# Optimization experiments

Hardware: AMD Instinct MI355X
Metric: run time of the kernel (lower is better)

The kernel has to match this reference:

```python
import jax, jax.numpy as jnp
import numpy as np

B, N, C = 2, 9216, 512
HEAD, SR = 8, 4
R = 32  # lora rank
SCALING = 4.0 / 32.0  # alpha / r


def setup_inputs() -> dict:
    key = jax.random.key(0)
    ks = jax.random.split(key, 16)
    s = 0.02
    inp = {
        "x": jax.random.normal(ks[0], (B, N, C), jnp.float32),
        "w_q": jax.random.normal(ks[1], (C, C), jnp.float32) * s,
        "b_q": jnp.zeros((C,), jnp.float32),
        "w_kv": jax.random.normal(ks[2], (2 * C, C), jnp.float32) * s,
        "b_kv": jnp.zeros((2 * C,), jnp.float32),
        "w_proj": jax.random.normal(ks[3], (C, C), jnp.float32) * s,
        "b_proj": jnp.zeros((C,), jnp.float32),
        "w_sr": jax.random.normal(ks[4], (C, C, SR, SR), jnp.float32) * s,
        "b_sr": jnp.zeros((C,), jnp.float32),
        "ln_g": jnp.ones((C,), jnp.float32),
        "ln_b": jnp.zeros((C,), jnp.float32),
        "lora_A_q": jax.random.normal(ks[5], (R, C), jnp.float32) * s,
        "lora_B_q": jax.random.normal(ks[6], (C, R), jnp.float32) * s,
        "lora_A_v": jax.random.normal(ks[7], (R, C), jnp.float32) * s,
        "lora_B_v": jax.random.normal(ks[8], (C, R), jnp.float32) * s,
        "H": 96,
        "W": 96,
    }
    return inp


def reference(x, w_q, b_q, w_kv, b_kv, w_proj, b_proj, w_sr, b_sr,
              ln_g, ln_b, lora_A_q, lora_B_q, lora_A_v, lora_B_v, H, W):
    b, n, c = x.shape
    d = c // HEAD
    # q = Linear(x) + LoRA(x) * scaling
    q = x @ w_q.T + b_q + ((x @ lora_A_q.T) @ lora_B_q.T) * SCALING
    q = q.reshape(b, n, HEAD, d).transpose(0, 2, 1, 3)  # (B, h, N, d)
    # spatial reduction: Conv2d(dim, dim, sr, sr) then LayerNorm
    xi = x.transpose(0, 2, 1).reshape(b, c, H, W)
    xs = jax.lax.conv_general_dilated(
        xi, w_sr, window_strides=(SR, SR), padding='VALID',
        dimension_numbers=('NCHW', 'OIHW', 'NCHW'))
    xs = xs + b_sr[None, :, None, None]
    xs = xs.reshape(b, c, -1).transpose(0, 2, 1)  # (B, Nkv, C)
    mu = jnp.mean(xs, axis=-1, keepdims=True)
    var = jnp.var(xs, axis=-1, keepdims=True)
    xs = (xs - mu) * jax.lax.rsqrt(var + 1e-5) * ln_g + ln_b
    # k, v
    kv = (xs @ w_kv.T + b_kv).reshape(b, -1, 2, HEAD, d).transpose(2, 0, 3, 1, 4)
    k, v = kv[0], kv[1]  # (B, h, Nkv, d)
    lv = ((xs @ lora_A_v.T) @ lora_B_v.T) * SCALING  # (B, Nkv, C)
    # faithful to torch: raw memory reshape, NOT a head-transpose
    v = v + lv.reshape(b, HEAD, -1, d)
    # attention
    attn = jax.nn.softmax(jnp.einsum('bhnd,bhmd->bhnm', q, k) * (d ** -0.5), axis=-1)
    out = jnp.einsum('bhnm,bhmd->bhnd', attn, v).transpose(0, 2, 1, 3).reshape(b, n, c)
    return out @ w_proj.T + b_proj
```

## Files before the change

### kernel.cpp

```cpp
#include <hip/hip_runtime.h>

typedef __attribute__((ext_vector_type(8))) __bf16 bf16x8;
typedef __attribute__((ext_vector_type(4))) float f32x4;
typedef __attribute__((ext_vector_type(4))) unsigned int u32x4;

#define MFMA16(a, b, c) __builtin_amdgcn_mfma_f32_16x16x32_bf16((a), (b), (c), 0, 0, 0)

__device__ __forceinline__ bool input_is_f32(const void* ln_g) {
    return ((const unsigned*)ln_g)[0] == 0x3F800000u;
}

__device__ __forceinline__ float rdf(const void* p, long i, bool f32) {
    return f32 ? ((const float*)p)[i] : (float)((const __bf16*)p)[i];
}

__device__ __forceinline__ void conv_big(const void* s, __bf16* d, long base, bool f) {
    long i = base + (long)threadIdx.x * 8;
    if (f) {
        f32x4 a = ((const f32x4*)s)[i / 4];
        f32x4 b = ((const f32x4*)s)[i / 4 + 1];
        bf16x8 o;
        #pragma unroll
        for (int j = 0; j < 4; ++j) { o[j] = (__bf16)a[j]; o[4 + j] = (__bf16)b[j]; }
        *(bf16x8*)(d + i) = o;
    } else {
        *(u32x4*)(d + i) = ((const u32x4*)s)[i / 8];
    }
}

__device__ __forceinline__ void conv_small(const void* s, __bf16* d, int n, bool f) {
    int i = threadIdx.x * 4;
    if (i < n) {
        #pragma unroll
        for (int j = 0; j < 4; ++j)
            d[i + j] = f ? (__bf16)((const float*)s)[i + j] : ((const __bf16*)s)[i + j];
    }
}

__global__ void convert_kernel(const void* x, const void* w_kv, const void* w_proj,
                               const void* b_q, const void* b_kv, const void* b_proj,
                               const void* b_sr, const void* ln_g, const void* ln_b,
                               __bf16* x_b, __bf16* w_kv_b, __bf16* w_proj_b,
                               __bf16* b_q_b, __bf16* b_kv_b, __bf16* b_proj_b,
                               __bf16* b_sr_b, __bf16* ln_g_b, __bf16* ln_b_b) {
    const bool f = input_is_f32(ln_g);
    int blk = blockIdx.x;
    if (blk < 4608)      conv_big(x, x_b, (long)blk * 2048, f);
    else if (blk < 4864) conv_big(w_kv, w_kv_b, (long)(blk - 4608) * 2048, f);
    else if (blk < 4992) conv_big(w_proj, w_proj_b, (long)(blk - 4864) * 2048, f);
    else if (blk == 4992) conv_small(b_q, b_q_b, 512, f);
    else if (blk == 4993) conv_small(b_kv, b_kv_b, 1024, f);
    else if (blk == 4994) conv_small(b_proj, b_proj_b, 512, f);
    else if (blk == 4995) conv_small(b_sr, b_sr_b, 512, f);
    else if (blk == 4996) conv_small(ln_g, ln_g_b, 512, f);
    else                  conv_small(ln_b, ln_b_b, 512, f);
}

__global__ void prep_kernel(const void* __restrict__ w_q,
                            const void* __restrict__ Aq, const void* __restrict__ Bq,
                            const void* __restrict__ Av, const void* __restrict__ Bv,
                            const void* __restrict__ w_sr, const void* __restrict__ ln_g,
                            __bf16* __restrict__ w_q_eff, __bf16* __restrict__ w_lv,
                            __bf16* __restrict__ w_sr_t) {
    const bool f = input_is_f32(ln_g);
    int tid = blockIdx.x * 256 + threadIdx.x;
    if (tid < 262144) {
        int o = tid >> 9, c = tid & 511;
        float acc = 0.f;
        #pragma unroll 8
        for (int r = 0; r < 32; ++r)
            acc += rdf(Bq, o * 32 + r, f) * rdf(Aq, r * 512 + c, f);
        w_q_eff[tid] = (__bf16)(rdf(w_q, tid, f) + 0.125f * acc);
    } else if (tid < 524288) {
        int t = tid - 262144;
        int o = t >> 9, c = t & 511;
        float acc = 0.f;
        #pragma unroll 8
        for (int r = 0; r < 32; ++r)
            acc += rdf(Bv, o * 32 + r, f) * rdf(Av, r * 512 + c, f);
        w_lv[t] = (__bf16)(0.125f * acc);
    } else if (tid < 786432) {
        int t = tid - 524288;
        int o = t >> 9, i = t & 511;
        #pragma unroll
        for (int p = 0; p < 16; ++p)
            w_sr_t[(size_t)o * 8192 + p * 512 + i] = (__bf16)rdf(w_sr, (long)t * 16 + p, f);
    }
}

__global__ __launch_bounds__(256) void gemm128(const __bf16* __restrict__ A,
                                               const __bf16* __restrict__ Bt,
                                               const __bf16* __restrict__ bias,
                                               void* __restrict__ out, int mode) {
    __shared__ __attribute__((aligned(16))) char lds[16384];
    char* As = lds;
    char* Bs = lds + 8192;
    const int tid = threadIdx.x;
    const int m0 = blockIdx.x << 7, n0 = blockIdx.y << 7;
    const int w = tid >> 6, lane = tid & 63;
    const int wm = (w >> 1) << 6, wn = (w & 1) << 6;
    const int lr = lane & 15, lg = lane >> 4;

    f32x4 acc[4][4] = {};

    const int srow = tid >> 1;
    const int sc0 = (tid & 1) * 2;
    const __bf16* Arow = A + (size_t)(m0 + srow) * 512;
    const __bf16* Brow = Bt + (size_t)(n0 + srow) * 512;

    for (int k0 = 0; k0 < 512; k0 += 32) {
        u32x4 a0 = *(const u32x4*)(Arow + k0 + sc0 * 8);
        u32x4 a1 = *(const u32x4*)(Arow + k0 + sc0 * 8 + 8);
        u32x4 b0 = *(const u32x4*)(Brow + k0 + sc0 * 8);
        u32x4 b1 = *(const u32x4*)(Brow + k0 + sc0 * 8 + 8);
        __syncthreads();
        *(u32x4*)(As + srow * 64 + sc0 * 16) = a0;
        *(u32x4*)(As + srow * 64 + sc0 * 16 + 16) = a1;
        *(u32x4*)(Bs + srow * 64 + sc0 * 16) = b0;
        *(u32x4*)(Bs + srow * 64 + sc0 * 16 + 16) = b1;
        __syncthreads();
        bf16x8 a[4], b[4];
        #pragma unroll
        for (int i = 0; i < 4; ++i)
            a[i] = *(const bf16x8*)(As + (wm + i * 16 + lr) * 64 + lg * 16);
        #pragma unroll
        for (int j = 0; j < 4; ++j)
            b[j] = *(const bf16x8*)(Bs + (wn + j * 16 + lr) * 64 + lg * 16);
        #pragma unroll
        for (int i = 0; i < 4; ++i)
            #pragma unroll
            for (int j = 0; j < 4; ++j)
                acc[i][j] = MFMA16(a[i], b[j], acc[i][j]);
    }

    #pragma unroll
    for (int j = 0; j < 4; ++j) {
        int col = n0 + wn + j * 16 + lr;
        float bv = (float)bias[col];
        #pragma unroll
        for (int i = 0; i < 4; ++i) {
            int rb = m0 + wm + i * 16 + lg * 4;
            #pragma unroll
            for (int r = 0; r < 4; ++r) {
                float v = acc[i][j][r] + bv;
                int grow = rb + r;
                if (mode == 0) {
                    ((float*)out)[(size_t)grow * 512 + col] = v;
                } else {
                    int b_ = grow >= 9216 ? 1 : 0;
                    int nn = grow - b_ * 9216;
                    ((__bf16*)out)[(((size_t)(b_ * 8 + (col >> 6))) * 9216 + nn) * 64 +
                                   (col & 63)] = (__bf16)v;
                }
            }
        }
    }
}

__global__ __launch_bounds__(256) void conv_gemm(const __bf16* __restrict__ x,
                                                 const __bf16* __restrict__ Wt,
                                                 float* __restrict__ part) {
    __shared__ __attribute__((aligned(16))) char lds[18432];
    char* As = lds;
    char* Bs = lds + 9216;
    const int tid = threadIdx.x;
    const int m0 = blockIdx.x << 6, n0 = blockIdx.y << 6;
    const int kz = blockIdx.z;
    const int kbase = kz << 10;
    const int w = tid >> 6, lane = tid & 63;
    const int wm = (w >> 1) << 5, wn = (w & 1) << 5;
    const int lr = lane & 15, lg = lane >> 4;

    const int srow = tid >> 2, sc = tid & 3;
    int m = m0 + srow;
    int bb = m >= 576 ? 1 : 0;
    int rem = m - bb * 576;
    int oy = rem / 24;
    int ox = rem - oy * 24;
    const __bf16* xrow = x + ((size_t)bb * 9216 + oy * 384 + ox * 4) * 512;
    const __bf16* brow = Wt + (size_t)(n0 + srow) * 8192;

    f32x4 acc[2][2] = {};
    for (int kk = 0; kk < 1024; kk += 64) {
        int k0 = kbase + kk;
        int p = k0 >> 9;
        int i0 = k0 & 511;
        int ky = p >> 2, kx = p & 3;
        const __bf16* xsrc = xrow + ((ky * 96 + kx) << 9) + i0;
        __syncthreads();
        #pragma unroll
        for (int j = 0; j < 2; ++j) {
            int c = sc + j * 4;
            u32x4 av = *(const u32x4*)(xsrc + c * 8);
            u32x4 bv = *(const u32x4*)(brow + k0 + c * 8);
            *(u32x4*)(As + srow * 144 + c * 16) = av;
            *(u32x4*)(Bs + srow * 144 + c * 16) = bv;
        }
        __syncthreads();
        bf16x8 a[2][2], b[2][2];
        #pragma unroll
        for (int i = 0; i < 2; ++i)
            #pragma unroll
            for (int ks = 0; ks < 2; ++ks) {
                a[i][ks] = *(const bf16x8*)(As + (wm + i * 16 + lr) * 144 + ks * 64 + lg * 16);
                b[i][ks] = *(const bf16x8*)(Bs + (wn + i * 16 + lr) * 144 + ks * 64 + lg * 16);
            }
        #pragma unroll
        for (int i = 0; i < 2; ++i)
            #pragma unroll
            for (int j = 0; j < 2; ++j)
                #pragma unroll
                for (int ks = 0; ks < 2; ++ks)
                    acc[i][j] = MFMA16(a[i][ks], b[j][ks], acc[i][j]);
    }
    float* pout = part + (size_t)kz * 589824;
    #pragma unroll
    for (int j = 0; j < 2; ++j) {
        int col = n0 + wn + j * 16 + lr;
        #pragma unroll
        for (int i = 0; i < 2; ++i) {
            int rb = m0 + wm + i * 16 + lg * 4;
            #pragma unroll
            for (int r = 0; r < 4; ++r)
                pout[(size_t)(rb + r) * 512 + col] = acc[i][j][r];
        }
    }
}

__global__ __launch_bounds__(64) void lnorm(const float* __restrict__ parts,
                                            const __bf16* __restrict__ b_sr,
                                            const __bf16* __restrict__ g,
                                            const __bf16* __restrict__ be,
                                            __bf16* __restrict__ out) {
    int row = blockIdx.x;
    int lane = threadIdx.x;
    const float* xr = parts + (size_t)row * 512;
    float v[8], s = 0.f, sq = 0.f;
    #pragma unroll
    for (int i = 0; i < 8; ++i) {
        int c = lane + i * 64;
        float t = (float)b_sr[c];
        #pragma unroll
        for (int sp = 0; sp < 8; ++sp)
            t += xr[(size_t)sp * 589824 + c];
        v[i] = t;
        s += t;
        sq += t * t;
    }
    #pragma unroll
    for (int d = 1; d < 64; d <<= 1) {
        s += __shfl_xor(s, d);
        sq += __shfl_xor(sq, d);
    }
    float mean = s * (1.0f / 512.0f);
    float var = sq * (1.0f / 512.0f) - mean * mean;
    float rstd = rsqrtf(var + 1e-5f);
    __bf16* orow = out + (size_t)row * 512;
    #pragma unroll
    for (int i = 0; i < 8; ++i) {
        int c = lane + i * 64;
        orow[c] = (__bf16)((v[i] - mean) * rstd * (float)g[c] + (float)be[c]);
    }
}

__global__ __launch_bounds__(256) void kv_gemm(const __bf16* __restrict__ xs,
                                               const __bf16* __restrict__ w_kv,
                                               const __bf16* __restrict__ w_lv,
                                               const __bf16* __restrict__ b_kv,
                                               __bf16* __restrict__ k_t,
                                               float* __restrict__ v_raw,
                                               __bf16* __restrict__ lv) {
    __shared__ __attribute__((aligned(16))) char lds[18432];
    char* As = lds;
    char* Bs = lds + 9216;
    const int tid = threadIdx.x;
    const int m0 = blockIdx.x << 6, n0 = blockIdx.y << 6;
    const int w = tid >> 6, lane = tid & 63;
    const int wm = (w >> 1) << 5, wn = (w & 1) << 5;
    const int lr = lane & 15, lg = lane >> 4;

    const int srow = tid >> 2, sc = tid & 3;
    const __bf16* arow = xs + (size_t)(m0 + srow) * 512;
    const __bf16* brow = (n0 < 1024) ? (w_kv + (size_t)(n0 + srow) * 512)
                                     : (w_lv + (size_t)(n0 - 1024 + srow) * 512);

    f32x4 acc[2][2] = {};
    for (int k0 = 0; k0 < 512; k0 += 64) {
        __syncthreads();
        #pragma unroll
        for (int j = 0; j < 2; ++j) {
            int c = sc + j * 4;
            u32x4 av = *(const u32x4*)(arow + k0 + c * 8);
            u32x4 bv = *(const u32x4*)(brow + k0 + c * 8);
            *(u32x4*)(As + srow * 144 + c * 16) = av;
            *(u32x4*)(Bs + srow * 144 + c * 16) = bv;
        }
        __syncthreads();
        bf16x8 a[2][2], b[2][2];
        #pragma unroll
        for (int i = 0; i < 2; ++i)
            #pragma unroll
            for (int ks = 0; ks < 2; ++ks) {
                a[i][ks] = *(const bf16x8*)(As + (wm + i * 16 + lr) * 144 + ks * 64 + lg * 16);
                b[i][ks] = *(const bf16x8*)(Bs + (wn + i * 16 + lr) * 144 + ks * 64 + lg * 16);
            }
        #pragma unroll
        for (int i = 0; i < 2; ++i)
            #pragma unroll
            for (int j = 0; j < 2; ++j)
                #pragma unroll
                for (int ks = 0; ks < 2; ++ks)
                    acc[i][j] = MFMA16(a[i][ks], b[j][ks], acc[i][j]);
    }
    #pragma unroll
    for (int j = 0; j < 2; ++j) {
        int col = n0 + wn + j * 16 + lr;
        float bv = (col < 1024) ? (float)b_kv[col] : 0.0f;
        #pragma unroll
        for (int i = 0; i < 2; ++i) {
            int rb = m0 + wm + i * 16 + lg * 4;
            #pragma unroll
            for (int r = 0; r < 4; ++r) {
                int grow = rb + r;
                float val = acc[i][j][r] + bv;
                int b_ = grow >= 576 ? 1 : 0;
                int mm = grow - b_ * 576;
                if (col < 512) {
                    int h = col >> 6, dd = col & 63;
                    k_t[(((size_t)(b_ * 8 + h)) * 576 + mm) * 64 + dd] = (__bf16)val;
                } else if (col < 1024) {
                    v_raw[((size_t)b_ * 576 + mm) * 512 + (col - 512)] = val;
                } else {
                    lv[((size_t)b_ * 576 + mm) * 512 + (col - 1024)] = (__bf16)val;
                }
            }
        }
    }
}

__global__ void v_fixup(const float* __restrict__ v_raw, const __bf16* __restrict__ lv,
                        __bf16* __restrict__ vT) {
    int tid = blockIdx.x * 256 + threadIdx.x;
    if (tid >= 589824) return;
    int mm = tid % 576;
    int rest = tid / 576;
    int dd = rest & 63;
    int bh = rest >> 6;
    int b_ = bh >> 3, h = bh & 7;
    int flat = h * 36864 + mm * 64 + dd;
    int n2 = flat >> 9, c2 = flat & 511;
    float val = v_raw[((size_t)b_ * 576 + mm) * 512 + h * 64 + dd] +
                (float)lv[((size_t)b_ * 576 + n2) * 512 + c2];
    vT[tid] = (__bf16)val;
}

__global__ __launch_bounds__(256) void attn_kernel(const __bf16* __restrict__ q_t,
                                                   const __bf16* __restrict__ k_t,
                                                   const __bf16* __restrict__ vT,
                                                   __bf16* __restrict__ attnv) {
    __shared__ __attribute__((aligned(16))) char lds[4608 + 5120 + 10240];
    char* Ks = lds;
    char* Vs = lds + 4608;
    char* Ps = lds + 9728;
    const int tid = threadIdx.x;
    const int w = tid >> 6, lane = tid & 63;
    const int lr = lane & 15, lg = lane >> 4;
    const int bh = blockIdx.y;
    const int qrow0 = (blockIdx.x << 7) + (w << 5);
    char* Psw = Ps + w * 2560;

    bf16x8 qf[2][2];
    #pragma unroll
    for (int mt = 0; mt < 2; ++mt)
        #pragma unroll
        for (int ks = 0; ks < 2; ++ks)
            qf[mt][ks] = *(const bf16x8*)(q_t + ((size_t)bh * 9216 + qrow0 + mt * 16 + lr) * 64 +
                                          ks * 32 + lg * 8);

    f32x4 oacc[2][4] = {};
    float lsum[2][4] = {};

    const int krow = tid >> 3, kc = tid & 7;
    const int vrow = tid >> 2, vc = tid & 3;

    for (int kv0 = 0; kv0 < 576; kv0 += 32) {
        __syncthreads();
        *(u32x4*)(Ks + krow * 144 + kc * 16) =
            *(const u32x4*)(k_t + ((size_t)bh * 576 + kv0 + krow) * 64 + kc * 8);
        *(u32x4*)(Vs + vrow * 80 + vc * 16) =
            *(const u32x4*)(vT + ((size_t)bh * 64 + vrow) * 576 + kv0 + vc * 8);
        __syncthreads();
        bf16x8 kf[2][2];
        #pragma unroll
        for (int nt = 0; nt < 2; ++nt)
            #pragma unroll
            for (int ks = 0; ks < 2; ++ks)
                kf[nt][ks] = *(const bf16x8*)(Ks + (nt * 16 + lr) * 144 + ks * 64 + lg * 16);
        f32x4 s[2][2] = {};
        #pragma unroll
        for (int mt = 0; mt < 2; ++mt)
            #pragma unroll
            for (int nt = 0; nt < 2; ++nt)
                #pragma unroll
                for (int ks = 0; ks < 2; ++ks)
                    s[mt][nt] = MFMA16(qf[mt][ks], kf[nt][ks], s[mt][nt]);
        #pragma unroll
        for (int mt = 0; mt < 2; ++mt)
            #pragma unroll
            for (int nt = 0; nt < 2; ++nt)
                #pragma unroll
                for (int r = 0; r < 4; ++r) {
                    float p = __expf(s[mt][nt][r] * 0.125f);
                    __bf16 pb = (__bf16)p;
                    lsum[mt][r] += (float)pb;
                    *(__bf16*)(Psw + (mt * 16 + lg * 4 + r) * 80 + (nt * 16 + lr) * 2) = pb;
                }
        __syncthreads();
        bf16x8 pf[2], vf[4];
        #pragma unroll
        for (int mt = 0; mt < 2; ++mt)
            pf[mt] = *(const bf16x8*)(Psw + (mt * 16 + lr) * 80 + lg * 16);
        #pragma unroll
        for (int nd = 0; nd < 4; ++nd)
            vf[nd] = *(const bf16x8*)(Vs + (nd * 16 + lr) * 80 + lg * 16);
        #pragma unroll
        for (int mt = 0; mt < 2; ++mt)
            #pragma unroll
            for (int nd = 0; nd < 4; ++nd)
                oacc[mt][nd] = MFMA16(pf[mt], vf[nd], oacc[mt][nd]);
    }

    #pragma unroll
    for (int mt = 0; mt < 2; ++mt)
        #pragma unroll
        for (int r = 0; r < 4; ++r) {
            float t = lsum[mt][r];
            t += __shfl_xor(t, 1);
            t += __shfl_xor(t, 2);
            t += __shfl_xor(t, 4);
            t += __shfl_xor(t, 8);
            lsum[mt][r] = 1.0f / t;
        }
    const int b_ = bh >> 3, h = bh & 7;
    #pragma unroll
    for (int mt = 0; mt < 2; ++mt)
        #pragma unroll
        for (int nd = 0; nd < 4; ++nd)
            #pragma unroll
            for (int r = 0; r < 4; ++r) {
                int row = qrow0 + mt * 16 + lg * 4 + r;
                int col = h * 64 + nd * 16 + lr;
                attnv[((size_t)b_ * 9216 + row) * 512 + col] =
                    (__bf16)(oacc[mt][nd][r] * lsum[mt][r]);
            }
}

extern "C" void kernel_launch(void* const* d_in, const int* in_sizes, int n_in,
                              void* d_out, int out_size, void* d_ws, size_t ws_size,
                              hipStream_t stream) {
    const void* x      = d_in[0];
    const void* w_q    = d_in[1];
    const void* b_q    = d_in[2];
    const void* w_kv   = d_in[3];
    const void* b_kv   = d_in[4];
    const void* w_proj = d_in[5];
    const void* b_proj = d_in[6];
    const void* w_sr   = d_in[7];
    const void* b_sr   = d_in[8];
    const void* ln_g   = d_in[9];
    const void* ln_b   = d_in[10];
    const void* A_q    = d_in[11];
    const void* B_q    = d_in[12];
    const void* A_v    = d_in[13];
    const void* B_v    = d_in[14];

    char* ws = (char*)d_ws;
    __bf16* x_b      = (__bf16*)(ws);
    __bf16* attnv    = (__bf16*)(ws);
    float*  parts    = (float*)(ws + 18874368);
    __bf16* q_t      = (__bf16*)(ws + 18874368);
    __bf16* k_t      = (__bf16*)(ws + 37748736);
    __bf16* vT       = (__bf16*)(ws + 38928384);
    __bf16* w_q_eff  = (__bf16*)(ws + 40108032);
    __bf16* w_lv     = (__bf16*)(ws + 40632320);
    __bf16* w_sr_t   = (__bf16*)(ws + 41156608);
    __bf16* w_kv_b   = (__bf16*)(ws + 49545216);
    __bf16* w_proj_b = (__bf16*)(ws + 50593792);
    __bf16* xs_ln    = (__bf16*)(ws + 53477376);
    float*  v_raw    = (float*)(ws + 54657024);
    __bf16* lv       = (__bf16*)(ws + 57016320);
    __bf16* b_q_b    = (__bf16*)(ws + 58195968);
    __bf16* b_kv_b   = (__bf16*)(ws + 58196992);
    __bf16* b_proj_b = (__bf16*)(ws + 58199040);
    __bf16* b_sr_b   = (__bf16*)(ws + 58200064);
    __bf16* ln_g_b   = (__bf16*)(ws + 58201088);
    __bf16* ln_b_b   = (__bf16*)(ws + 58202112);

    convert_kernel<<<4998, 256, 0, stream>>>(x, w_kv, w_proj, b_q, b_kv, b_proj,
                                             b_sr, ln_g, ln_b,
                                             x_b, w_kv_b, w_proj_b, b_q_b, b_kv_b,
                                             b_proj_b, b_sr_b, ln_g_b, ln_b_b);
    prep_kernel<<<3072, 256, 0, stream>>>(w_q, A_q, B_q, A_v, B_v, w_sr, ln_g,
                                          w_q_eff, w_lv, w_sr_t);
    conv_gemm<<<dim3(18, 8, 8), 256, 0, stream>>>(x_b, w_sr_t, parts);
    lnorm<<<1152, 64, 0, stream>>>(parts, b_sr_b, ln_g_b, ln_b_b, xs_ln);
    gemm128<<<dim3(144, 4), 256, 0, stream>>>(x_b, w_q_eff, b_q_b, q_t, 1);
    kv_gemm<<<dim3(18, 24), 256, 0, stream>>>(xs_ln, w_kv_b, w_lv, b_kv_b, k_t, v_raw, lv);
    v_fixup<<<2304, 256, 0, stream>>>(v_raw, lv, vT);
    attn_kernel<<<dim3(72, 16), 256, 0, stream>>>(q_t, k_t, vT, attnv);
    gemm128<<<dim3(144, 4), 256, 0, stream>>>(attnv, w_proj_b, b_proj_b, d_out, 0);
}
```

Before: 287.6 us.

## Keep softmax probabilities in registers via transposed QK MFMA and fold scale into Q

The attention kernel now computes S^T (K as the A operand, Q as B) so the exponentiated scores land in registers already laid out as the A operand of the PV MFMA. This removes the LDS round-trip for P and one barrier per tile. Row sums are accumulated with an extra MFMA against a ones vector, which replaces the shuffle reduction. The KV tile grows to 64 with global loads issued before the barrier, V is stored with a permuted layout to match the new P fragment ordering, and the softmax scale times log2(e) is folded into Q at the GEMM epilogue so the kernel can use a raw exp2. This changes bf16 rounding of Q slightly.

```diff
diff --git a/kernel.cpp b/kernel.cpp
--- a/kernel.cpp
+++ b/kernel.cpp
@@ -3,8 +3,10 @@
 typedef __attribute__((ext_vector_type(8))) __bf16 bf16x8;
 typedef __attribute__((ext_vector_type(4))) float f32x4;
 typedef __attribute__((ext_vector_type(4))) unsigned int u32x4;
+typedef __attribute__((ext_vector_type(2))) unsigned int u32x2;
 
 #define MFMA16(a, b, c) __builtin_amdgcn_mfma_f32_16x16x32_bf16((a), (b), (c), 0, 0, 0)
+#define QSCALE 0.18033688011112042f
 
 __device__ __forceinline__ bool input_is_f32(const void* ln_g) {
     return ((const unsigned*)ln_g)[0] == 0x3F800000u;
@@ -150,7 +152,7 @@
                     int b_ = grow >= 9216 ? 1 : 0;
                     int nn = grow - b_ * 9216;
                     ((__bf16*)out)[(((size_t)(b_ * 8 + (col >> 6))) * 9216 + nn) * 64 +
-                                   (col & 63)] = (__bf16)v;
+                                   (col & 63)] = (__bf16)(v * QSCALE);
                 }
             }
         }
@@ -358,101 +360,109 @@
                                                    const __bf16* __restrict__ k_t,
                                                    const __bf16* __restrict__ vT,
                                                    __bf16* __restrict__ attnv) {
-    __shared__ __attribute__((aligned(16))) char lds[4608 + 5120 + 10240];
+    __shared__ __attribute__((aligned(16))) char lds[18432];
     char* Ks = lds;
-    char* Vs = lds + 4608;
-    char* Ps = lds + 9728;
+    char* Vs = lds + 9216;
     const int tid = threadIdx.x;
     const int w = tid >> 6, lane = tid & 63;
     const int lr = lane & 15, lg = lane >> 4;
     const int bh = blockIdx.y;
     const int qrow0 = (blockIdx.x << 7) + (w << 5);
-    char* Psw = Ps + w * 2560;
 
     bf16x8 qf[2][2];
     #pragma unroll
-    for (int mt = 0; mt < 2; ++mt)
+    for (int qb = 0; qb < 2; ++qb)
         #pragma unroll
         for (int ks = 0; ks < 2; ++ks)
-            qf[mt][ks] = *(const bf16x8*)(q_t + ((size_t)bh * 9216 + qrow0 + mt * 16 + lr) * 64 +
+            qf[qb][ks] = *(const bf16x8*)(q_t + ((size_t)bh * 9216 + qrow0 + qb * 16 + lr) * 64 +
                                           ks * 32 + lg * 8);
 
+    bf16x8 ones;
+    #pragma unroll
+    for (int j = 0; j < 8; ++j) ones[j] = (__bf16)1.0f;
+
     f32x4 oacc[2][4] = {};
-    float lsum[2][4] = {};
-
-    const int krow = tid >> 3, kc = tid & 7;
-    const int vrow = tid >> 2, vc = tid & 3;
-
-    for (int kv0 = 0; kv0 < 576; kv0 += 32) {
-        __syncthreads();
-        *(u32x4*)(Ks + krow * 144 + kc * 16) =
-            *(const u32x4*)(k_t + ((size_t)bh * 576 + kv0 + krow) * 64 + kc * 8);
-        *(u32x4*)(Vs + vrow * 80 + vc * 16) =
-            *(const u32x4*)(vT + ((size_t)bh * 64 + vrow) * 576 + kv0 + vc * 8);
-        __syncthreads();
-        bf16x8 kf[2][2];
-        #pragma unroll
-        for (int nt = 0; nt < 2; ++nt)
-            #pragma unroll
-            for (int ks = 0; ks < 2; ++ks)
-                kf[nt][ks] = *(const bf16x8*)(Ks + (nt * 16 + lr) * 144 + ks * 64 + lg * 16);
-        f32x4 s[2][2] = {};
-        #pragma unroll
-        for (int mt = 0; mt < 2; ++mt)
-            #pragma unroll
-            for (int nt = 0; nt < 2; ++nt)
+    f32x4 lacc[2] = {};
+
+    const int rr = tid >> 2, q4 = tid & 3;
+    const __bf16* kg = k_t + ((size_t)bh * 576 + rr) * 64 + q4 * 16;
+    char* ksw = Ks + rr * 144 + q4 * 32;
+    const __bf16* vg = vT + ((size_t)bh * 64 + rr) * 576 + q4 * 16;
+    char* vsw = Vs + rr * 144;
+    const int offA = ((q4 & 1) << 3) | ((q4 >> 1) << 6);
+
+    for (int kv0 = 0; kv0 < 576; kv0 += 64) {
+        u32x4 k0v = *(const u32x4*)(kg + (size_t)kv0 * 64);
+        u32x4 k1v = *(const u32x4*)(kg + (size_t)kv0 * 64 + 8);
+        u32x4 v0v = *(const u32x4*)(vg + kv0);
+        u32x4 v1v = *(const u32x4*)(vg + kv0 + 8);
+        __syncthreads();
+        *(u32x4*)(ksw) = k0v;
+        *(u32x4*)(ksw + 16) = k1v;
+        u32x2 t0, t1, t2, t3;
+        t0[0] = v0v[0]; t0[1] = v0v[1];
+        t1[0] = v0v[2]; t1[1] = v0v[3];
+        t2[0] = v1v[0]; t2[1] = v1v[1];
+        t3[0] = v1v[2]; t3[1] = v1v[3];
+        *(u32x2*)(vsw + offA) = t0;
+        *(u32x2*)(vsw + offA + 16) = t1;
+        *(u32x2*)(vsw + offA + 32) = t2;
+        *(u32x2*)(vsw + offA + 48) = t3;
+        __syncthreads();
+
+        #pragma unroll
+        for (int ch = 0; ch < 2; ++ch) {
+            bf16x8 kf[2][2];
+            #pragma unroll
+            for (int kb = 0; kb < 2; ++kb)
                 #pragma unroll
                 for (int ks = 0; ks < 2; ++ks)
-                    s[mt][nt] = MFMA16(qf[mt][ks], kf[nt][ks], s[mt][nt]);
-        #pragma unroll
-        for (int mt = 0; mt < 2; ++mt)
-            #pragma unroll
-            for (int nt = 0; nt < 2; ++nt)
+                    kf[kb][ks] = *(const bf16x8*)(Ks + ((ch * 2 + kb) * 16 + lr) * 144 +
+                                                  ks * 64 + lg * 16);
+            f32x4 st[2][2] = {};
+            #pragma unroll
+            for (int kb = 0; kb < 2; ++kb)
                 #pragma unroll
-                for (int r = 0; r < 4; ++r) {
-                    float p = __expf(s[mt][nt][r] * 0.125f);
-                    __bf16 pb = (__bf16)p;
-                    lsum[mt][r] += (float)pb;
-                    *(__bf16*)(Psw + (mt * 16 + lg * 4 + r) * 80 + (nt * 16 + lr) * 2) = pb;
-                }
-        __syncthreads();
-        bf16x8 pf[2], vf[4];
-        #pragma unroll
-        for (int mt = 0; mt < 2; ++mt)
-            pf[mt] = *(const bf16x8*)(Psw + (mt * 16 + lr) * 80 + lg * 16);
+                for (int qb = 0; qb < 2; ++qb)
+                    #pragma unroll
+                    for (int ks = 0; ks < 2; ++ks)
+                        st[kb][qb] = MFMA16(kf[kb][ks], qf[qb][ks], st[kb][qb]);
+            bf16x8 vf[4];
+            #pragma unroll
+            for (int nd = 0; nd < 4; ++nd)
+                vf[nd] = *(const bf16x8*)(Vs + (nd * 16 + lr) * 144 + ch * 64 + lg * 16);
+            #pragma unroll
+            for (int qb = 0; qb < 2; ++qb) {
+                bf16x8 pa;
+                #pragma unroll
+                for (int kb = 0; kb < 2; ++kb)
+                    #pragma unroll
+                    for (int r = 0; r < 4; ++r)
+                        pa[kb * 4 + r] = (__bf16)__builtin_amdgcn_exp2f(st[kb][qb][r]);
+                #pragma unroll
+                for (int nd = 0; nd < 4; ++nd)
+                    oacc[qb][nd] = MFMA16(pa, vf[nd], oacc[qb][nd]);
+                lacc[qb] = MFMA16(pa, ones, lacc[qb]);
+            }
+        }
+    }
+
+    const int b_ = bh >> 3, h = bh & 7;
+    #pragma unroll
+    for (int qb = 0; qb < 2; ++qb) {
+        f32x4 linv;
+        #pragma unroll
+        for (int r = 0; r < 4; ++r) linv[r] = 1.0f / lacc[qb][r];
         #pragma unroll
         for (int nd = 0; nd < 4; ++nd)
-            vf[nd] = *(const bf16x8*)(Vs + (nd * 16 + lr) * 80 + lg * 16);
-        #pragma unroll
-        for (int mt = 0; mt < 2; ++mt)
-            #pragma unroll
-            for (int nd = 0; nd < 4; ++nd)
-                oacc[mt][nd] = MFMA16(pf[mt], vf[nd], oacc[mt][nd]);
-    }
-
-    #pragma unroll
-    for (int mt = 0; mt < 2; ++mt)
-        #pragma unroll
-        for (int r = 0; r < 4; ++r) {
-            float t = lsum[mt][r];
-            t += __shfl_xor(t, 1);
-            t += __shfl_xor(t, 2);
-            t += __shfl_xor(t, 4);
-            t += __shfl_xor(t, 8);
-            lsum[mt][r] = 1.0f / t;
-        }
-    const int b_ = bh >> 3, h = bh & 7;
-    #pragma unroll
-    for (int mt = 0; mt < 2; ++mt)
-        #pragma unroll
-        for (int nd = 0; nd < 4; ++nd)
             #pragma unroll
             for (int r = 0; r < 4; ++r) {
-                int row = qrow0 + mt * 16 + lg * 4 + r;
+                int row = qrow0 + qb * 16 + lg * 4 + r;
                 int col = h * 64 + nd * 16 + lr;
                 attnv[((size_t)b_ * 9216 + row) * 512 + col] =
-                    (__bf16)(oacc[mt][nd][r] * lsum[mt][r]);
+                    (__bf16)(oacc[qb][nd][r] * linv[r]);
             }
+    }
 }
 
 extern "C" void kernel_launch(void* const* d_in, const int* in_sizes, int n_in,
```

Result: faster. 269.9 us (-6.1%).
